# Kernel optimization log

Hardware: AMD Instinct MI355X
Metric: run time of the kernel (lower is better)

## Reference

```python
import jax, jax.numpy as jnp
import numpy as np

H = 768
W = 768
N = 64


def setup_inputs() -> dict:
    key = jax.random.key(0)
    k1, k2, k3 = jax.random.split(key, 3)
    img = jax.random.normal(k1, (H, W, 3), dtype=jnp.float32)
    # control points lie inside the image
    pi = jax.random.uniform(k2, (N, 2), dtype=jnp.float32, minval=0.0, maxval=float(min(W, H)))
    qi = pi + 20.0 * jax.random.normal(k3, (N, 2), dtype=jnp.float32)
    return {"img": img, "pi": pi, "qi": qi}


def reference(img, pi, qi):
    # MLS rigid deformation (Schaefer et al.). Returns dense remap grid (H, W, 2).
    h, w = img.shape[0], img.shape[1]
    n = pi.shape[0]
    pi = pi.astype(jnp.float32)
    qi = qi.astype(jnp.float32)

    # v[x, y] = (x, y); matches torch coordinate_buffer[0:W, 0:H]
    xs = jnp.arange(w, dtype=jnp.float32)
    ys = jnp.arange(h, dtype=jnp.float32)
    v = jnp.stack(jnp.meshgrid(xs, ys, indexing="ij"), axis=-1)  # (W, H, 2)

    # inverse-square-distance weights, (W, H, N)
    d2 = jnp.sum((pi[None, None, :, :] - v[:, :, None, :]) ** 2, axis=-1)
    wgt = 1.0 / (d2 + 1e-9)
    sw = jnp.sum(wgt, axis=2, keepdims=True)  # (W, H, 1)

    pstar = jnp.matmul(wgt, pi) / sw  # (W, H, 2) weighted centroid of pi
    qstar = jnp.matmul(wgt, qi) / sw  # (W, H, 2) weighted centroid of qi

    phat = pi[None, None, :, :] - pstar[:, :, None, :]  # (W, H, N, 2)
    qhat = qi[None, None, :, :] - qstar[:, :, None, :]  # (W, H, N, 2)

    vp = v - pstar  # (W, H, 2)
    vp_perp = jnp.stack((vp[..., 1], -vp[..., 0]), axis=-1)            # (W, H, 2)
    phat_perp = jnp.stack((phat[..., 1], -phat[..., 0]), axis=-1)      # (W, H, N, 2)

    # Entries of the 2x2 similarity blocks A_n = w_n * [[a, b], [c, d]] computed
    # as fused contractions instead of materializing (W, H, N, 2, 2).
    a = jnp.einsum("whnc,whc->whn", phat, vp)
    b = jnp.einsum("whnc,whc->whn", phat, vp_perp)
    c = jnp.einsum("whnc,whc->whn", phat_perp, vp)
    d = jnp.einsum("whnc,whc->whn", phat_perp, vp_perp)

    # frv = sum_n qhat_n (1x2) @ A_n (2x2)
    frv_x = jnp.sum(wgt * (qhat[..., 0] * a + qhat[..., 1] * c), axis=2)
    frv_y = jnp.sum(wgt * (qhat[..., 0] * b + qhat[..., 1] * d), axis=2)
    frv = jnp.stack((frv_x, frv_y), axis=-1)  # (W, H, 2)

    vp_norm = jnp.linalg.norm(vp, axis=-1, keepdims=True)          # (W, H, 1)
    frv_norm = jnp.linalg.norm(frv, axis=-1, keepdims=True) + 1e-10
    fv = vp_norm * frv / frv_norm + qstar                           # (W, H, 2)

    return jnp.transpose(fv, (1, 0, 2))  # (H, W, 2)
```

## Files before the change

kernel.cpp:

```cpp
#include <hip/hip_runtime.h>


#define IMG_H 768
#define IMG_W 768
#define NPTS 64

__device__ __forceinline__ float rdlane(float v, int lane) {
    return __int_as_float(__builtin_amdgcn_readlane(__float_as_int(v), lane));
}

__device__ __forceinline__ float2 mls_finish(
    float vxk, float vy,
    float sw, float spx, float spy, float sqx, float sqy,
    float sre, float sim)
{
    const float rsw = __builtin_amdgcn_rcpf(sw);
    const float psx = spx * rsw, psy = spy * rsw;
    const float qsx = sqx * rsw, qsy = sqy * rsw;
    const float cre = fmaf(sqx, spx, sqy * spy) * rsw;
    const float cim = fmaf(sqy, spx, -sqx * spy) * rsw;
    const float Sre = sre - cre;
    const float Sim = sim - cim;
    const float vpx = vxk - psx;
    const float vpy = vy - psy;
    const float frx = fmaf(vpx, Sre, -vpy * Sim);
    const float fry = fmaf(vpx, Sim, vpy * Sre);
    const float vpn = sqrtf(fmaf(vpx, vpx, vpy * vpy));
    const float frn = sqrtf(fmaf(frx, frx, fry * fry)) + 1e-10f;
    const float s = vpn * __builtin_amdgcn_rcpf(frn);
    return make_float2(fmaf(s, frx, qsx), fmaf(s, fry, qsy));
}

__global__ __launch_bounds__(256) void mls_main(
    const float* __restrict__ pi,
    const float* __restrict__ qi,
    float* __restrict__ out)
{
    const int tid  = threadIdx.x;
    const int lane = tid & 63;

    const float2 p = ((const float2*)pi)[lane];
    const float2 q = ((const float2*)qi)[lane];
    const float lpx = p.x, lpy = p.y, lqx = q.x, lqy = q.y;
    const float lcre = fmaf(q.x, p.x,  q.y * p.y);
    const float lcim = fmaf(q.y, p.x, -q.x * p.y);

    const int y = blockIdx.x;
    const float vy = (float)y;
    const float vx = (float)(3 * tid);

    float sw0 = 0.f, spx0 = 0.f, spy0 = 0.f, sqx0 = 0.f, sqy0 = 0.f, sre0 = 0.f, sim0 = 0.f;
    float sw1 = 0.f, spx1 = 0.f, spy1 = 0.f, sqx1 = 0.f, sqy1 = 0.f, sre1 = 0.f, sim1 = 0.f;
    float sw2 = 0.f, spx2 = 0.f, spy2 = 0.f, sqx2 = 0.f, sqy2 = 0.f, sre2 = 0.f, sim2 = 0.f;

    #pragma unroll
    for (int n = 0; n < NPTS; ++n) {
        const float px  = rdlane(lpx,  n);
        const float py  = rdlane(lpy,  n);
        const float qx  = rdlane(lqx,  n);
        const float qy  = rdlane(lqy,  n);
        const float cre = rdlane(lcre, n);
        const float cim = rdlane(lcim, n);

        const float dx = px - vx;
        const float dy = py - vy;
        const float t  = fmaf(dy, dy, 1e-9f);
        const float d0 = fmaf(dx, dx, t);
        const float d1 = fmaf(-2.f, dx, d0) + 1.0f;
        const float d2 = fmaf(-4.f, dx, d0) + 4.0f;
        const float w0 = __builtin_amdgcn_rcpf(d0);
        const float w1 = __builtin_amdgcn_rcpf(d1);
        const float w2 = __builtin_amdgcn_rcpf(d2);

        sw0  += w0;                   sw1  += w1;                   sw2  += w2;
        spx0 = fmaf(w0, px,  spx0);   spx1 = fmaf(w1, px,  spx1);   spx2 = fmaf(w2, px,  spx2);
        spy0 = fmaf(w0, py,  spy0);   spy1 = fmaf(w1, py,  spy1);   spy2 = fmaf(w2, py,  spy2);
        sqx0 = fmaf(w0, qx,  sqx0);   sqx1 = fmaf(w1, qx,  sqx1);   sqx2 = fmaf(w2, qx,  sqx2);
        sqy0 = fmaf(w0, qy,  sqy0);   sqy1 = fmaf(w1, qy,  sqy1);   sqy2 = fmaf(w2, qy,  sqy2);
        sre0 = fmaf(w0, cre, sre0);   sre1 = fmaf(w1, cre, sre1);   sre2 = fmaf(w2, cre, sre2);
        sim0 = fmaf(w0, cim, sim0);   sim1 = fmaf(w1, cim, sim1);   sim2 = fmaf(w2, cim, sim2);
    }

    const float2 r0 = mls_finish(vx,       vy, sw0, spx0, spy0, sqx0, sqy0, sre0, sim0);
    const float2 r1 = mls_finish(vx + 1.f, vy, sw1, spx1, spy1, sqx1, sqy1, sre1, sim1);
    const float2 r2 = mls_finish(vx + 2.f, vy, sw2, spx2, spy2, sqx2, sqy2, sre2, sim2);

    float2* orow = (float2*)out + (size_t)y * IMG_W + 3 * tid;
    orow[0] = r0;
    orow[1] = r1;
    orow[2] = r2;
}

extern "C" void kernel_launch(void* const* d_in, const int* in_sizes, int n_in,
                              void* d_out, int out_size, void* d_ws, size_t ws_size,
                              hipStream_t stream) {
    const float* pi = (const float*)d_in[1];
    const float* qi = (const float*)d_in[2];
    float* out = (float*)d_out;

    mls_main<<<IMG_H, 256, 0, stream>>>(pi, qi, out);
}
```

Before: 19.33 us.

## Compute two pixels per thread over a flat grid, with scalar control-point loads

```diff
diff --git a/kernel.cpp b/kernel.cpp
--- a/kernel.cpp
+++ b/kernel.cpp
@@ -10,17 +10,15 @@
 }
 
 __device__ __forceinline__ float2 mls_finish(
-    float vxk, float vy,
-    float sw, float spx, float spy, float sqx, float sqy,
+    float vxk, float vy, float sw,
+    float spx, float spy, float sqx, float sqy,
     float sre, float sim)
 {
     const float rsw = __builtin_amdgcn_rcpf(sw);
     const float psx = spx * rsw, psy = spy * rsw;
     const float qsx = sqx * rsw, qsy = sqy * rsw;
-    const float cre = fmaf(sqx, spx, sqy * spy) * rsw;
-    const float cim = fmaf(sqy, spx, -sqx * spy) * rsw;
-    const float Sre = sre - cre;
-    const float Sim = sim - cim;
+    const float Sre = fmaf(sw, sre, -fmaf(sqx, spx,  sqy * spy));
+    const float Sim = fmaf(sw, sim, -fmaf(sqy, spx, -sqx * spy));
     const float vpx = vxk - psx;
     const float vpy = vy - psy;
     const float frx = fmaf(vpx, Sre, -vpy * Sim);
@@ -36,29 +34,29 @@
     const float* __restrict__ qi,
     float* __restrict__ out)
 {
-    const int tid  = threadIdx.x;
+    const int tid = threadIdx.x;
     const int lane = tid & 63;
 
-    const float2 p = ((const float2*)pi)[lane];
-    const float2 q = ((const float2*)qi)[lane];
-    const float lpx = p.x, lpy = p.y, lqx = q.x, lqy = q.y;
-    const float lcre = fmaf(q.x, p.x,  q.y * p.y);
-    const float lcim = fmaf(q.y, p.x, -q.x * p.y);
+    const float2 lp = ((const float2*)pi)[lane];
+    const float2 lq = ((const float2*)qi)[lane];
+    const float lcre = fmaf(lq.x, lp.x,  lq.y * lp.y);
+    const float lcim = fmaf(lq.y, lp.x, -lq.x * lp.y);
 
-    const int y = blockIdx.x;
+    const int idx = blockIdx.x * 256 + tid;
+    const int xh = idx % (IMG_W / 2);
+    const int y  = idx / (IMG_W / 2);
+    const float vx = (float)(2 * xh);
     const float vy = (float)y;
-    const float vx = (float)(3 * tid);
 
     float sw0 = 0.f, spx0 = 0.f, spy0 = 0.f, sqx0 = 0.f, sqy0 = 0.f, sre0 = 0.f, sim0 = 0.f;
     float sw1 = 0.f, spx1 = 0.f, spy1 = 0.f, sqx1 = 0.f, sqy1 = 0.f, sre1 = 0.f, sim1 = 0.f;
-    float sw2 = 0.f, spx2 = 0.f, spy2 = 0.f, sqx2 = 0.f, sqy2 = 0.f, sre2 = 0.f, sim2 = 0.f;
 
     #pragma unroll
     for (int n = 0; n < NPTS; ++n) {
-        const float px  = rdlane(lpx,  n);
-        const float py  = rdlane(lpy,  n);
-        const float qx  = rdlane(lqx,  n);
-        const float qy  = rdlane(lqy,  n);
+        const float px = pi[2 * n + 0];
+        const float py = pi[2 * n + 1];
+        const float qx = qi[2 * n + 0];
+        const float qy = qi[2 * n + 1];
         const float cre = rdlane(lcre, n);
         const float cim = rdlane(lcim, n);
 
@@ -67,28 +65,22 @@
         const float t  = fmaf(dy, dy, 1e-9f);
         const float d0 = fmaf(dx, dx, t);
         const float d1 = fmaf(-2.f, dx, d0) + 1.0f;
-        const float d2 = fmaf(-4.f, dx, d0) + 4.0f;
         const float w0 = __builtin_amdgcn_rcpf(d0);
         const float w1 = __builtin_amdgcn_rcpf(d1);
-        const float w2 = __builtin_amdgcn_rcpf(d2);
 
-        sw0  += w0;                   sw1  += w1;                   sw2  += w2;
-        spx0 = fmaf(w0, px,  spx0);   spx1 = fmaf(w1, px,  spx1);   spx2 = fmaf(w2, px,  spx2);
-        spy0 = fmaf(w0, py,  spy0);   spy1 = fmaf(w1, py,  spy1);   spy2 = fmaf(w2, py,  spy2);
-        sqx0 = fmaf(w0, qx,  sqx0);   sqx1 = fmaf(w1, qx,  sqx1);   sqx2 = fmaf(w2, qx,  sqx2);
-        sqy0 = fmaf(w0, qy,  sqy0);   sqy1 = fmaf(w1, qy,  sqy1);   sqy2 = fmaf(w2, qy,  sqy2);
-        sre0 = fmaf(w0, cre, sre0);   sre1 = fmaf(w1, cre, sre1);   sre2 = fmaf(w2, cre, sre2);
-        sim0 = fmaf(w0, cim, sim0);   sim1 = fmaf(w1, cim, sim1);   sim2 = fmaf(w2, cim, sim2);
+        sw0  += w0;                   sw1  += w1;
+        spx0 = fmaf(w0, px,  spx0);   spx1 = fmaf(w1, px,  spx1);
+        spy0 = fmaf(w0, py,  spy0);   spy1 = fmaf(w1, py,  spy1);
+        sqx0 = fmaf(w0, qx,  sqx0);   sqx1 = fmaf(w1, qx,  sqx1);
+        sqy0 = fmaf(w0, qy,  sqy0);   sqy1 = fmaf(w1, qy,  sqy1);
+        sre0 = fmaf(w0, cre, sre0);   sre1 = fmaf(w1, cre, sre1);
+        sim0 = fmaf(w0, cim, sim0);   sim1 = fmaf(w1, cim, sim1);
     }
 
     const float2 r0 = mls_finish(vx,       vy, sw0, spx0, spy0, sqx0, sqy0, sre0, sim0);
     const float2 r1 = mls_finish(vx + 1.f, vy, sw1, spx1, spy1, sqx1, sqy1, sre1, sim1);
-    const float2 r2 = mls_finish(vx + 2.f, vy, sw2, spx2, spy2, sqx2, sqy2, sre2, sim2);
 
-    float2* orow = (float2*)out + (size_t)y * IMG_W + 3 * tid;
-    orow[0] = r0;
-    orow[1] = r1;
-    orow[2] = r2;
+    ((float4*)out)[idx] = make_float4(r0.x, r0.y, r1.x, r1.y);
 }
 
 extern "C" void kernel_launch(void* const* d_in, const int* in_sizes, int n_in,
@@ -98,5 +90,6 @@
     const float* qi = (const float*)d_in[2];
     float* out = (float*)d_out;
 
-    mls_main<<<IMG_H, 256, 0, stream>>>(pi, qi, out);
+    const int nthreads = IMG_H * (IMG_W / 2);
+    mls_main<<<nthreads / 256, 256, 0, stream>>>(pi, qi, out);
 }
```

Result: no change. 19.56 us (median of 2 runs) (+1.2%).
